# Optimization experiments

Hardware: AMD Instinct MI355X
Metric: run time of the kernel (lower is better)

Reference implementation:

```python
import jax, jax.numpy as jnp
import numpy as np

V = 32000; D = 128; L = 2048; B = 4
DI = 256; DS = 16; K = 4; H = 4; NM = 6; NA = 2; PAD = 0


def setup_inputs() -> dict:
    key = jax.random.key(0)
    ks = jax.random.split(key, 24)
    n = lambda i, shape, s: jax.random.normal(ks[i], shape, dtype=jnp.float32) * s
    inp = {}
    inp["input_ids"] = jax.random.randint(ks[0], (B, L), 0, V)
    inp["token_types"] = jax.random.randint(ks[1], (B, L), 0, 10)
    inp["timestamps"] = jax.random.uniform(ks[2], (B, L), dtype=jnp.float32)
    inp["emb"] = n(3, (V, D), 0.02).at[PAD].set(0.0)
    inp["type_emb"] = n(4, (10, D), 0.02)
    inp["te_freqs"] = n(5, (D // 2,), 0.1)
    inp["te_phases"] = jnp.zeros((D // 2,), jnp.float32)
    inp["te_w"] = n(6, (D, D), 0.05)
    inp["te_b"] = jnp.zeros((D,), jnp.float32)
    # Mamba blocks (stacked over NM)
    inp["m_norm_w"] = jnp.ones((NM, D), jnp.float32)
    inp["m_norm_b"] = jnp.zeros((NM, D), jnp.float32)
    inp["m_in_w"] = n(7, (NM, 2 * DI, D), 0.05)
    inp["m_conv_w"] = n(8, (NM, DI, 1, K), 0.2)   # depthwise, OIH with I=1
    inp["m_conv_b"] = jnp.zeros((NM, DI), jnp.float32)
    inp["m_dt_w"] = n(9, (NM, DI, DI), 0.05)
    inp["m_dt_b"] = jnp.zeros((NM, DI), jnp.float32)
    inp["m_B_w"] = n(10, (NM, DS, DI), 0.05)
    inp["m_C_w"] = n(11, (NM, DS, DI), 0.05)
    inp["m_D"] = jnp.ones((NM, DI), jnp.float32)
    inp["m_A_log"] = jnp.broadcast_to(jnp.log(jnp.arange(1, DS + 1, dtype=jnp.float32)), (NM, DI, DS)) + 0.0
    inp["m_out_w"] = n(12, (NM, D, DI), 0.05)
    # Attention blocks (stacked over NA)
    inp["a_ln1_w"] = jnp.ones((NA, D), jnp.float32)
    inp["a_ln1_b"] = jnp.zeros((NA, D), jnp.float32)
    inp["a_qkv_w"] = n(13, (NA, 3 * D, D), 0.05)
    inp["a_qkv_b"] = jnp.zeros((NA, 3 * D), jnp.float32)
    inp["a_out_w"] = n(14, (NA, D, D), 0.05)
    inp["a_out_b"] = jnp.zeros((NA, D), jnp.float32)
    inp["a_ln2_w"] = jnp.ones((NA, D), jnp.float32)
    inp["a_ln2_b"] = jnp.zeros((NA, D), jnp.float32)
    inp["a_f1_w"] = n(15, (NA, 4 * D, D), 0.05)
    inp["a_f1_b"] = jnp.zeros((NA, 4 * D), jnp.float32)
    inp["a_f2_w"] = n(16, (NA, D, 4 * D), 0.05)
    inp["a_f2_b"] = jnp.zeros((NA, D), jnp.float32)
    # Task head (n_tasks=1)
    inp["h_ln_w"] = jnp.ones((D,), jnp.float32)
    inp["h_ln_b"] = jnp.zeros((D,), jnp.float32)
    inp["h_w"] = n(17, (1, D), 0.05)
    inp["h_b"] = jnp.zeros((1,), jnp.float32)
    return inp


def _ln(x, w, b, eps=1e-5):
    mu = x.mean(-1, keepdims=True)
    var = ((x - mu) ** 2).mean(-1, keepdims=True)
    return (x - mu) * jax.lax.rsqrt(var + eps) * w + b


def _mamba(x, nw, nb, inw, cw, cb, dtw, dtb, bw, cpw, Dp, Alog, ow):
    res = x
    xn = _ln(x, nw, nb)
    xz = xn @ inw.T                              # [B,L,2*DI]
    xp, z = jnp.split(xz, 2, axis=-1)
    # causal depthwise conv: left-pad K-1, take first L outputs
    xc = jax.lax.conv_general_dilated(
        xp.transpose(0, 2, 1), cw, (1,), [(K - 1, 0)],
        feature_group_count=DI, dimension_numbers=("NCH", "OIH", "NCH"))
    xc = (xc + cb[None, :, None]).transpose(0, 2, 1)
    xc = jax.nn.silu(xc)
    dt = jax.nn.softplus(xc @ dtw.T + dtb)       # [B,L,DI]
    Bm = xc @ bw.T                               # [B,L,DS]
    Cm = xc @ cpw.T                              # [B,L,DS]
    A = -jnp.exp(Alog)                           # [DI,DS]

    def step(h, inp):
        dt_t, x_t, b_t, c_t = inp                # [B,DI],[B,DI],[B,DS],[B,DS]
        h = h * jnp.exp(A * dt_t[..., None]) + (x_t * dt_t)[..., None] * b_t[:, None, :]
        return h, (h * c_t[:, None, :]).sum(-1)

    xs = (jnp.moveaxis(dt, 1, 0), jnp.moveaxis(xc, 1, 0),
          jnp.moveaxis(Bm, 1, 0), jnp.moveaxis(Cm, 1, 0))
    h0 = jnp.zeros((x.shape[0], DI, DS), x.dtype)
    _, y = jax.lax.scan(step, h0, xs)            # y: [L,B,DI]
    y = jnp.moveaxis(y, 0, 1)
    y = y + xc * Dp
    y = y * jax.nn.silu(z)
    return res + y @ ow.T


def _attn(x, l1w, l1b, qkvw, qkvb, ow, ob, l2w, l2b, f1w, f1b, f2w, f2b):
    res = x
    xn = _ln(x, l1w, l1b)
    qkv = xn @ qkvw.T + qkvb
    q, k, v = jnp.split(qkv, 3, axis=-1)
    dh = D // H
    rs = lambda t: t.reshape(t.shape[0], t.shape[1], H, dh)
    q, k, v = rs(q), rs(k), rs(v)
    sc = jnp.einsum("bqhd,bkhd->bhqk", q, k) / jnp.sqrt(jnp.float32(dh))
    p = jax.nn.softmax(sc, axis=-1)
    o = jnp.einsum("bhqk,bkhd->bqhd", p, v).reshape(x.shape)
    x = res + o @ ow.T + ob
    ff = jax.nn.gelu(_ln(x, l2w, l2b) @ f1w.T + f1b, approximate=False) @ f2w.T + f2b
    return x + ff


def reference(input_ids, token_types, timestamps, emb, type_emb, te_freqs, te_phases, te_w, te_b,
              m_norm_w, m_norm_b, m_in_w, m_conv_w, m_conv_b, m_dt_w, m_dt_b, m_B_w, m_C_w,
              m_D, m_A_log, m_out_w,
              a_ln1_w, a_ln1_b, a_qkv_w, a_qkv_b, a_out_w, a_out_b, a_ln2_w, a_ln2_b,
              a_f1_w, a_f1_b, a_f2_w, a_f2_b, h_ln_w, h_ln_b, h_w, h_b):
    t = timestamps[..., None]
    enc = jnp.concatenate([jnp.sin(t * te_freqs + te_phases),
                           jnp.cos(t * te_freqs + te_phases)], axis=-1)
    x = emb[input_ids] + type_emb[token_types] + enc @ te_w.T + te_b
    attn_every = (NM + NA) // NA
    mi = 0; ai = 0
    for i in range(NM + NA):
        if (i + 1) % attn_every == 0:
            x = _attn(x, a_ln1_w[ai], a_ln1_b[ai], a_qkv_w[ai], a_qkv_b[ai],
                      a_out_w[ai], a_out_b[ai], a_ln2_w[ai], a_ln2_b[ai],
                      a_f1_w[ai], a_f1_b[ai], a_f2_w[ai], a_f2_b[ai])
            ai += 1
        else:
            x = _mamba(x, m_norm_w[mi], m_norm_b[mi], m_in_w[mi], m_conv_w[mi], m_conv_b[mi],
                       m_dt_w[mi], m_dt_b[mi], m_B_w[mi], m_C_w[mi], m_D[mi], m_A_log[mi], m_out_w[mi])
            mi += 1
    cls = x[:, 0, :]
    return (_ln(cls, h_ln_w, h_ln_b) @ h_w.T + h_b)[:, 0]
```

## Files before the change

### kernel.cpp

```cpp
#include <hip/hip_runtime.h>
#include <hip/hip_bf16.h>
#include <math.h>

constexpr int Ll = 2048, Bb = 4, DIi = 256, Hh = 4;
constexpr int TOK = Bb * Ll;
constexpr int NC = 128;
constexpr int CH = 16;
constexpr float LOG2E = 1.442695040888963f;

#define DEV __device__ __forceinline__

DEV float siluf(float v)     { return v / (1.f + expf(-v)); }
DEV float softplusf(float v) { return (v > 20.f) ? v : log1pf(expf(v)); }
DEV float geluf(float v)     { return 0.5f * v * (1.f + erff(v * 0.7071067811865476f)); }

#if defined(__has_builtin)
#if __has_builtin(__builtin_amdgcn_exp2f)
#define EXP2F __builtin_amdgcn_exp2f
#endif
#endif
#ifndef EXP2F
#define EXP2F exp2f
#endif

DEV short f2bf(float f) {
    union { float f; unsigned u; } a; a.f = f;
    unsigned r = (a.u + 0x7fffu + ((a.u >> 16) & 1u)) >> 16;
    return (short)r;
}

using bf16x8 = __attribute__((ext_vector_type(8))) short;
using f16x8  = __attribute__((ext_vector_type(8))) _Float16;
using f32x4  = __attribute__((ext_vector_type(4))) float;

__global__ __launch_bounds__(256) void wprep_kernel(
    const float* s0, const float* s1, const float* s2, const float* s3,
    const float* s4, const float* s5, const float* s6, const float* s7,
    const float* s8, const float* s9, _Float16* dst)
{
    constexpr int base[10] = {0, 16384, 409600, 802816, 827392, 851968,
                              1048576, 1146880, 1179648, 1310720};
    constexpr int nseg[10] = {16384, 393216, 393216, 24576, 24576, 196608,
                              98304, 32768, 131072, 131072};
    int seg = blockIdx.y;
    int t = blockIdx.x * 256 + threadIdx.x;
    if (t >= nseg[seg]) return;
    const float* src;
    switch (seg) {
        case 0: src = s0; break; case 1: src = s1; break;
        case 2: src = s2; break; case 3: src = s3; break;
        case 4: src = s4; break; case 5: src = s5; break;
        case 6: src = s6; break; case 7: src = s7; break;
        case 8: src = s8; break; default: src = s9; break;
    }
    dst[base[seg] + t] = (_Float16)src[t];
}

__global__ __launch_bounds__(256) void gather_enc_kernel(
    const int* __restrict__ ids, const int* __restrict__ tts,
    const float* __restrict__ ts, const float* __restrict__ emb,
    const float* __restrict__ temb, const float* __restrict__ freqs,
    const float* __restrict__ phases, float* __restrict__ x,
    float* __restrict__ enc)
{
    int tok = blockIdx.x * 2 + (threadIdx.x >> 7);
    int d = threadIdx.x & 127;
    float tval = ts[tok];
    int j = d & 63;
    float a = tval * freqs[j] + phases[j];
    enc[(size_t)tok * 128 + d] = (d < 64) ? sinf(a) : cosf(a);
    int id = ids[tok];
    int tt = tts[tok];
    x[(size_t)tok * 128 + d] = emb[(size_t)id * 128 + d] + temb[(size_t)tt * 128 + d];
}

__global__ __launch_bounds__(256) void ln_stats_kernel(
    const float* __restrict__ x, float2* __restrict__ stats)
{
    int wid = threadIdx.x >> 6, lane = threadIdx.x & 63;
    int tok = blockIdx.x * 4 + wid;
    float2 v = *(const float2*)(x + (size_t)tok * 128 + lane * 2);
    float s = v.x + v.y, sq = v.x * v.x + v.y * v.y;
#pragma unroll
    for (int o = 32; o > 0; o >>= 1) { s += __shfl_xor(s, o); sq += __shfl_xor(sq, o); }
    if (lane == 0) {
        float mu = s * (1.f / 128.f);
        float var = sq * (1.f / 128.f) - mu * mu;
        stats[tok] = make_float2(mu, rsqrtf(var + 1e-5f));
    }
}

template <int ACT, bool BIAS, bool ADD, bool LNA, int MODE>
__global__ __launch_bounds__(256) void gemm64_kernel(
    const float* __restrict__ A, const _Float16* __restrict__ W,
    const float* __restrict__ bias, float* __restrict__ C,
    const float* __restrict__ lnw, const float* __restrict__ lnb,
    const float2* __restrict__ stats,
    const _Float16* __restrict__ Bw, const _Float16* __restrict__ Cw,
    float* __restrict__ bmo, float* __restrict__ cmo,
    short* __restrict__ kbf, short* __restrict__ vbf,
    int M, int N, int Kd, int lda, int ldc)
{
    __shared__ _Float16 As[64][72];
    __shared__ _Float16 Ws[64][72];
    const int by = blockIdx.y;
    const bool isBC = (MODE == 1) && (by == (int)gridDim.y - 1);
    const int bm0 = blockIdx.x * 64, bn0 = by * 64;
    const int tid = threadIdx.x;
    const int w = tid >> 6, l = tid & 63;
    const int wr = w >> 1, wc = w & 1;
    const int fr = l & 15, fk = (l >> 4) * 8;
    const int srow = tid >> 2, skc = (tid & 3) * 16;
    float mu = 0.f, rstd = 1.f;
    if (LNA) { float2 st = stats[bm0 + srow]; mu = st.x; rstd = st.y; }
    f32x4 acc[2][2] = {};

    for (int k0 = 0; k0 < Kd; k0 += 64) {
        const float* ap = A + (size_t)(bm0 + srow) * lda + k0 + skc;
        const _Float16* wp;
        if (isBC) {
            if (srow < 16)      wp = Bw + (size_t)srow * Kd + k0 + skc;
            else if (srow < 32) wp = Cw + (size_t)(srow - 16) * Kd + k0 + skc;
            else                wp = Bw + k0 + skc;
        } else {
            wp = W + (size_t)(bn0 + srow) * Kd + k0 + skc;
        }
        float af[16];
#pragma unroll
        for (int q = 0; q < 4; q++)
            *(float4*)(af + q * 4) = *(const float4*)(ap + q * 4);
        f16x8 wb0 = *(const f16x8*)wp;
        f16x8 wb1 = *(const f16x8*)(wp + 8);
        if (LNA) {
#pragma unroll
            for (int q = 0; q < 4; q++) {
                float4 w4 = *(const float4*)(lnw + k0 + skc + q * 4);
                float4 b4 = *(const float4*)(lnb + k0 + skc + q * 4);
                af[q*4+0] = (af[q*4+0] - mu) * rstd * w4.x + b4.x;
                af[q*4+1] = (af[q*4+1] - mu) * rstd * w4.y + b4.y;
                af[q*4+2] = (af[q*4+2] - mu) * rstd * w4.z + b4.z;
                af[q*4+3] = (af[q*4+3] - mu) * rstd * w4.w + b4.w;
            }
        }
        f16x8 ab0, ab1;
#pragma unroll
        for (int q = 0; q < 8; q++) {
            ab0[q] = (_Float16)af[q]; ab1[q] = (_Float16)af[q + 8];
        }
        __syncthreads();
        *(f16x8*)&As[srow][skc]     = ab0;
        *(f16x8*)&As[srow][skc + 8] = ab1;
        *(f16x8*)&Ws[srow][skc]     = wb0;
        *(f16x8*)&Ws[srow][skc + 8] = wb1;
        __syncthreads();
#pragma unroll
        for (int ks = 0; ks < 64; ks += 32) {
            f16x8 afr0 = *(const f16x8*)&As[wr * 32 + fr][ks + fk];
            f16x8 afr1 = *(const f16x8*)&As[wr * 32 + 16 + fr][ks + fk];
            f16x8 wfr0 = *(const f16x8*)&Ws[wc * 32 + fr][ks + fk];
            f16x8 wfr1 = *(const f16x8*)&Ws[wc * 32 + 16 + fr][ks + fk];
            acc[0][0] = __builtin_amdgcn_mfma_f32_16x16x32_f16(afr0, wfr0, acc[0][0], 0, 0, 0);
            acc[0][1] = __builtin_amdgcn_mfma_f32_16x16x32_f16(afr0, wfr1, acc[0][1], 0, 0, 0);
            acc[1][0] = __builtin_amdgcn_mfma_f32_16x16x32_f16(afr1, wfr0, acc[1][0], 0, 0, 0);
            acc[1][1] = __builtin_amdgcn_mfma_f32_16x16x32_f16(afr1, wfr1, acc[1][1], 0, 0, 0);
        }
    }
#pragma unroll
    for (int ri = 0; ri < 2; ri++)
#pragma unroll
    for (int ci = 0; ci < 2; ci++) {
        const int lcol = wc * 32 + ci * 16 + fr;
        const int col = bn0 + lcol;
        const int row0 = bm0 + wr * 32 + ri * 16 + (l >> 4) * 4;
        if (isBC) {
            if (lcol < 32) {
                float* dst = (lcol < 16) ? bmo : cmo;
                const int cc = lcol & 15;
#pragma unroll
                for (int r = 0; r < 4; r++)
                    dst[(size_t)(row0 + r) * 16 + cc] = acc[ri][ci][r];
            }
        } else if (MODE == 2) {
            const float bv = bias[col];
            const int b = row0 >> 11, tl0 = row0 & 2047;
            if (col < 128) {
#pragma unroll
                for (int r = 0; r < 4; r++)
                    C[(size_t)(row0 + r) * 128 + col] = acc[ri][ci][r] + bv;
            } else if (col < 256) {
                const int hc = col - 128;
                short* kp = kbf + ((size_t)(b * 4 + (hc >> 5)) * 2048 + tl0) * 32 + (hc & 31);
#pragma unroll
                for (int r = 0; r < 4; r++)
                    kp[(size_t)r * 32] = f2bf(acc[ri][ci][r] + bv);
            } else {
                const int hc = col - 256;
                short4 vk;
#pragma unroll
                for (int r = 0; r < 4; r++)
                    ((short*)&vk)[r] = f2bf(acc[ri][ci][r] + bv);
                *(short4*)(vbf + ((size_t)(b * 4 + (hc >> 5)) * 32 + (hc & 31)) * 2048 + tl0) = vk;
            }
        } else {
            const float bv = BIAS ? bias[col] : 0.f;
#pragma unroll
            for (int r = 0; r < 4; r++) {
                float t = acc[ri][ci][r] + bv;
                if (ACT == 1) t = softplusf(t);
                if (ACT == 2) t = geluf(t);
                float* p = C + (size_t)(row0 + r) * ldc + col;
                if (ADD) t += *p;
                *p = t;
            }
        }
    }
}

__global__ __launch_bounds__(256) void conv_kernel(
    const float* __restrict__ xz, const float* __restrict__ cw,
    const float* __restrict__ cb, float* __restrict__ xc)
{
    int g = blockIdx.x * 256 + threadIdx.x;
    int c = g & 255;
    int t = (g >> 8) & 2047;
    int b = g >> 19;
    float4 w4 = *(const float4*)(cw + (size_t)c * 4);
    float acc = cb[c];
    const float* base = xz + ((size_t)b * 2048 + t) * 512 + c;
    if (t >= 3) {
        acc += base[-3 * 512] * w4.x + base[-2 * 512] * w4.y + base[-512] * w4.z + base[0] * w4.w;
    } else {
        const float wv[4] = {w4.x, w4.y, w4.z, w4.w};
#pragma unroll
        for (int kk = 0; kk < 4; kk++) {
            int tt = t - 3 + kk;
            if (tt >= 0) acc += xz[((size_t)b * 2048 + tt) * 512 + c] * wv[kk];
        }
    }
    xc[g] = siluf(acc);
}

__global__ __launch_bounds__(256) void scan1_kernel(
    const float* __restrict__ dt, const float* __restrict__ xc,
    const float* __restrict__ bm, const float* __restrict__ Alog,
    float* __restrict__ F, float* __restrict__ sumdt)
{
    int c = threadIdx.x;
    int k = blockIdx.x & (NC - 1);
    int b = blockIdx.x / NC;
    __shared__ float sB[CH][16];
    int t0 = k * CH;
    if (threadIdx.x < CH * 4) {
        int r = threadIdx.x >> 2, c4 = (threadIdx.x & 3) << 2;
        *(float4*)&sB[r][c4] = *(const float4*)(bm + ((size_t)b * 2048 + t0 + r) * 16 + c4);
    }
    float A2[16];
#pragma unroll
    for (int s = 0; s < 16; s++) A2[s] = -expf(Alog[(size_t)c * 16 + s]) * LOG2E;
    __syncthreads();
    float h[16] = {};
    float sd = 0.f;
    size_t base = ((size_t)b * 2048 + t0) * 256 + c;
    for (int tt = 0; tt < CH; tt++) {
        float d  = dt[base + (size_t)tt * 256];
        float xv = xc[base + (size_t)tt * 256];
        sd += d;
        float xdt = xv * d;
#pragma unroll
        for (int s = 0; s < 16; s++) h[s] = h[s] * EXP2F(A2[s] * d) + xdt * sB[tt][s];
    }
    size_t fo = (((size_t)b * NC + k) * 256 + c) * 16;
#pragma unroll
    for (int s = 0; s < 16; s += 4) *(float4*)(F + fo + s) = make_float4(h[s], h[s+1], h[s+2], h[s+3]);
    sumdt[((size_t)b * NC + k) * 256 + c] = sd;
}

__global__ __launch_bounds__(256) void scan2_kernel(
    float* __restrict__ F, const float* __restrict__ sumdt,
    const float* __restrict__ Alog)
{
    int g = blockIdx.x * 256 + threadIdx.x;
    int s = g & 15, c = (g >> 4) & 255, b = g >> 12;
    float A2 = -expf(Alog[(size_t)c * 16 + s]) * LOG2E;
    float h = 0.f;
    for (int k = 0; k < NC; k++) {
        size_t o = (((size_t)b * NC + k) * 256 + c) * 16 + s;
        float tmp = F[o];
        F[o] = h;
        h = h * EXP2F(A2 * sumdt[((size_t)b * NC + k) * 256 + c]) + tmp;
    }
}

__global__ __launch_bounds__(256) void scan3_kernel(
    const float* __restrict__ dt, const float* __restrict__ xc,
    const float* __restrict__ bm, const float* __restrict__ cm,
    const float* __restrict__ xz, const float* __restrict__ Alog,
    const float* __restrict__ Dp, const float* __restrict__ Hs,
    float* __restrict__ y)
{
    int c = threadIdx.x;
    int k = blockIdx.x & (NC - 1);
    int b = blockIdx.x / NC;
    __shared__ float sB[CH][16], sC[CH][16];
    int t0 = k * CH;
    if (threadIdx.x < CH * 4) {
        int r = threadIdx.x >> 2, c4 = (threadIdx.x & 3) << 2;
        *(float4*)&sB[r][c4] = *(const float4*)(bm + ((size_t)b * 2048 + t0 + r) * 16 + c4);
        *(float4*)&sC[r][c4] = *(const float4*)(cm + ((size_t)b * 2048 + t0 + r) * 16 + c4);
    }
    float A2[16];
#pragma unroll
    for (int s = 0; s < 16; s++) A2[s] = -expf(Alog[(size_t)c * 16 + s]) * LOG2E;
    __syncthreads();
    float h[16];
    size_t ho = (((size_t)b * NC + k) * 256 + c) * 16;
#pragma unroll
    for (int s = 0; s < 16; s++) h[s] = Hs[ho + s];
    float Dv = Dp[c];
    size_t base  = ((size_t)b * 2048 + t0) * 256 + c;
    size_t zbase = ((size_t)b * 2048 + t0) * 512 + 256 + c;
    for (int tt = 0; tt < CH; tt++) {
        float d  = dt[base + (size_t)tt * 256];
        float xv = xc[base + (size_t)tt * 256];
        float xdt = xv * d;
        float yv = 0.f;
#pragma unroll
        for (int s = 0; s < 16; s++) {
            h[s] = h[s] * EXP2F(A2[s] * d) + xdt * sB[tt][s];
            yv += h[s] * sC[tt][s];
        }
        yv += xv * Dv;
        float zv = xz[zbase + (size_t)tt * 512];
        y[base + (size_t)tt * 256] = yv * siluf(zv);
    }
}

__global__ __launch_bounds__(256) void attn_part_kernel(
    const float* __restrict__ qbuf, const short* __restrict__ kbf,
    const short* __restrict__ vbf, float* __restrict__ pO, float* __restrict__ pml)
{
    __shared__ short Klds[2][64 * 32];
    __shared__ short Vlds[2][32 * 64];
    __shared__ short Pt[4][64][18];
    const int qt = blockIdx.x, b = blockIdx.z;
    const int h = blockIdx.y >> 2, sp = blockIdx.y & 3;
    const int tid = threadIdx.x;
    const int w = tid >> 6, l = tid & 63;
    const int q16 = l & 15, g = l >> 4;
    const float cQ = 0.25503634043f;

    const int qrow = qt * 64 + w * 16 + q16;
    const float* qp = qbuf + ((size_t)(b * 2048 + qrow)) * 128 + 32 * h + g * 8;
    bf16x8 qfrag;
    {
        float qf[8];
        *(float4*)qf       = *(const float4*)qp;
        *(float4*)(qf + 4) = *(const float4*)(qp + 4);
#pragma unroll
        for (int i = 0; i < 8; i++) qfrag[i] = f2bf(qf[i] * cQ);
    }
    const int bh = b * 4 + h;
    const short* kb = kbf + ((size_t)bh * 2048) * 32;
    const short* vb = vbf + ((size_t)bh * 32) * 2048;

    const int vrow = tid >> 3;
    const int vsw  = ((tid & 7) * 16) ^ ((vrow & 7) << 4);
    const int ts0 = sp * 8;

    bf16x8 kst, vst;
    auto ldregs = [&](int t) {
        kst = *(const bf16x8*)(kb + (size_t)t * 2048 + tid * 8);
        vst = *(const bf16x8*)(vb + (size_t)vrow * 2048 + t * 64 + (vsw >> 1));
    };
    auto dswrite = [&](int buf) {
        *(bf16x8*)&Klds[buf][tid * 8] = kst;
        *(bf16x8*)&Vlds[buf][tid * 8] = vst;
    };

    float m = -1e30f, lsum = 0.f;
    f32x4 O0 = {0.f, 0.f, 0.f, 0.f}, O1 = {0.f, 0.f, 0.f, 0.f};
    const f32x4 zf = {0.f, 0.f, 0.f, 0.f};

    auto step = [&](int buf) {
        bf16x8 kf[4];
#pragma unroll
        for (int kt = 0; kt < 4; kt++)
            kf[kt] = *(const bf16x8*)&Klds[buf][(kt * 16 + q16) * 32 + g * 8];
        f32x4 St[4];
#pragma unroll
        for (int kt = 0; kt < 4; kt++)
            St[kt] = __builtin_amdgcn_mfma_f32_16x16x32_bf16(kf[kt], qfrag, zf, 0, 0, 0);
        float pm = St[0][0];
#pragma unroll
        for (int kt = 0; kt < 4; kt++)
#pragma unroll
            for (int r = 0; r < 4; r++) pm = fmaxf(pm, St[kt][r]);
        pm = fmaxf(pm, __shfl_xor(pm, 16));
        pm = fmaxf(pm, __shfl_xor(pm, 32));
        float mn = fmaxf(m, pm);
        float rs = EXP2F(m - mn);
        float ps = 0.f;
#pragma unroll
        for (int kt = 0; kt < 4; kt++)
#pragma unroll
            for (int r = 0; r < 4; r++) {
                float p = EXP2F(St[kt][r] - mn);
                ps += p;
                Pt[w][kt * 16 + g * 4 + r][q16] = f2bf(p);
            }
        ps += __shfl_xor(ps, 16);
        ps += __shfl_xor(ps, 32);
        lsum = lsum * rs + ps;
        m = mn;
        O0 *= rs; O1 *= rs;
#pragma unroll
        for (int c = 0; c < 2; c++) {
            bf16x8 pb;
#pragma unroll
            for (int i = 0; i < 8; i++) pb[i] = Pt[w][c * 32 + g * 8 + i][q16];
#pragma unroll
            for (int hf = 0; hf < 2; hf++) {
                const int d = q16 + 16 * hf;
                bf16x8 vf = *(const bf16x8*)&Vlds[buf][d * 64 + ((c * 32 + g * 8) ^ ((d & 7) << 3))];
                if (hf == 0) O0 = __builtin_amdgcn_mfma_f32_16x16x32_bf16(vf, pb, O0, 0, 0, 0);
                else         O1 = __builtin_amdgcn_mfma_f32_16x16x32_bf16(vf, pb, O1, 0, 0, 0);
            }
        }
    };

    ldregs(ts0);
    dswrite(0);
    ldregs(ts0 + 1);
    int cur = 0;
    for (int i = 0; i < 8; i++) {
        __syncthreads();
        if (i + 1 < 8) {
            dswrite(cur ^ 1);
            if (i + 2 < 8) ldregs(ts0 + i + 2);
        }
        step(cur);
        cur ^= 1;
    }

    size_t po = (((size_t)(bh * 4 + sp)) * 2048 + qrow) * 32;
#pragma unroll
    for (int r = 0; r < 4; r++) {
        pO[po + g * 4 + r]      = O0[r];
        pO[po + 16 + g * 4 + r] = O1[r];
    }
    if (g == 0) {
        size_t mo = (((size_t)(bh * 4 + sp)) * 2048 + qrow) * 2;
        pml[mo]     = m;
        pml[mo + 1] = lsum;
    }
}

__global__ __launch_bounds__(256) void attn_comb_kernel(
    const float* __restrict__ pO, const float* __restrict__ pml,
    float* __restrict__ aout)
{
    int gid = blockIdx.x * 256 + threadIdx.x;
    int d = gid & 31, q = (gid >> 5) & 2047, bh = gid >> 16;
    float m[4], lv[4], M = -1e30f;
#pragma unroll
    for (int s = 0; s < 4; s++) {
        size_t mo = (((size_t)(bh * 4 + s)) * 2048 + q) * 2;
        m[s] = pml[mo]; lv[s] = pml[mo + 1];
        M = fmaxf(M, m[s]);
    }
    float L = 0.f, o = 0.f;
#pragma unroll
    for (int s = 0; s < 4; s++) {
        float wgt = EXP2F(m[s] - M);
        L += lv[s] * wgt;
        o += pO[(((size_t)(bh * 4 + s)) * 2048 + q) * 32 + d] * wgt;
    }
    int b = bh >> 2, h = bh & 3;
    aout[((size_t)(b * 2048 + q)) * 128 + h * 32 + d] = o / L;
}

__global__ __launch_bounds__(128) void head_kernel(
    const float* __restrict__ x, const float* __restrict__ w,
    const float* __restrict__ bsp, const float* __restrict__ hw,
    const float* __restrict__ hb, float* __restrict__ out)
{
    int bb = blockIdx.x;
    int d = threadIdx.x;
    int wid = d >> 6, lane = d & 63;
    float v = x[(size_t)bb * 2048 * 128 + d];
    float s = v, sq = v * v;
#pragma unroll
    for (int o = 32; o > 0; o >>= 1) { s += __shfl_xor(s, o); sq += __shfl_xor(sq, o); }
    __shared__ float red[4];
    if (lane == 0) { red[wid] = s; red[2 + wid] = sq; }
    __syncthreads();
    s = red[0] + red[1]; sq = red[2] + red[3];
    float mu = s * (1.f / 128.f);
    float var = sq * (1.f / 128.f) - mu * mu;
    float xn = (v - mu) * rsqrtf(var + 1e-5f) * w[d] + bsp[d];
    float pr = xn * hw[d];
#pragma unroll
    for (int o = 32; o > 0; o >>= 1) pr += __shfl_xor(pr, o);
    __syncthreads();
    if (lane == 0) red[wid] = pr;
    __syncthreads();
    if (d == 0) out[bb] = red[0] + red[1] + hb[0];
}

constexpr size_t OFF_X  = 0;
constexpr size_t OFF_XZ = (size_t)1 << 20;
constexpr size_t OFF_XC = (size_t)5 << 20;
constexpr size_t OFF_DT = (size_t)7 << 20;
constexpr size_t OFF_Y  = (size_t)9 << 20;
constexpr size_t OFF_BM = (size_t)11 << 20;
constexpr size_t OFF_CM = OFF_BM + 131072;
constexpr size_t OFF_SD = OFF_CM + 131072;
constexpr size_t OFF_ST = OFF_SD + 131072;
constexpr size_t OFF_F  = OFF_ST + 16384;
constexpr size_t OFF_WF = OFF_F + ((size_t)2 << 20);
constexpr size_t WS_FLOATS = OFF_WF + 720896;

extern "C" void kernel_launch(void* const* d_in, const int* in_sizes, int n_in,
                              void* d_out, int out_size, void* d_ws, size_t ws_size,
                              hipStream_t stream)
{
    const int*   ids   = (const int*)d_in[0];
    const int*   tts   = (const int*)d_in[1];
    const float* tstmp = (const float*)d_in[2];
    const float* emb   = (const float*)d_in[3];
    const float* temb  = (const float*)d_in[4];
    const float* tef   = (const float*)d_in[5];
    const float* tep   = (const float*)d_in[6];
    const float* tew   = (const float*)d_in[7];
    const float* tebi  = (const float*)d_in[8];
    const float* mnw   = (const float*)d_in[9];
    const float* mnb   = (const float*)d_in[10];
    const float* minw  = (const float*)d_in[11];
    const float* mcwp  = (const float*)d_in[12];
    const float* mcb   = (const float*)d_in[13];
    const float* mdtw  = (const float*)d_in[14];
    const float* mdtb  = (const float*)d_in[15];
    const float* mbw   = (const float*)d_in[16];
    const float* mcw2  = (const float*)d_in[17];
    const float* mD    = (const float*)d_in[18];
    const float* mAl   = (const float*)d_in[19];
    const float* mow   = (const float*)d_in[20];
    const float* al1w  = (const float*)d_in[21];
    const float* al1b  = (const float*)d_in[22];
    const float* aqkvw = (const float*)d_in[23];
    const float* aqkvb = (const float*)d_in[24];
    const float* aow   = (const float*)d_in[25];
    const float* aob   = (const float*)d_in[26];
    const float* al2w  = (const float*)d_in[27];
    const float* al2b  = (const float*)d_in[28];
    const float* af1w  = (const float*)d_in[29];
    const float* af1b  = (const float*)d_in[30];
    const float* af2w  = (const float*)d_in[31];
    const float* af2b  = (const float*)d_in[32];
    const float* hlnw  = (const float*)d_in[33];
    const float* hlnb  = (const float*)d_in[34];
    const float* hw    = (const float*)d_in[35];
    const float* hb    = (const float*)d_in[36];
    float* out = (float*)d_out;
    float* wsf = (float*)d_ws;
    if (ws_size < WS_FLOATS * sizeof(float)) return;

    float* x    = wsf + OFF_X;
    float* xz   = wsf + OFF_XZ;
    float* xc   = wsf + OFF_XC;
    float* dtb  = wsf + OFF_DT;
    float* yb   = wsf + OFF_Y;
    float* bm   = wsf + OFF_BM;
    float* cm   = wsf + OFF_CM;
    float* sdb  = wsf + OFF_SD;
    float2* stats = (float2*)(wsf + OFF_ST);
    float* Fb   = wsf + OFF_F;
    float* ff   = xz;
    float* aout = yb;
    float* qbuf = xc;
    float* pO   = xz;
    float* pml  = dtb;
    float* encb = Fb;
    short* kbf  = (short*)(wsf + OFF_F);
    short* vbf  = (short*)(wsf + OFF_F + ((size_t)1 << 20));
    _Float16* wf16 = (_Float16*)(wsf + OFF_WF);

    const _Float16* tew16   = wf16;
    const _Float16* minw16  = wf16 + 16384;
    const _Float16* mdtw16  = wf16 + 409600;
    const _Float16* mbw16   = wf16 + 802816;
    const _Float16* mcw216  = wf16 + 827392;
    const _Float16* mow16   = wf16 + 851968;
    const _Float16* aqkvw16 = wf16 + 1048576;
    const _Float16* aow16   = wf16 + 1146880;
    const _Float16* af1w16  = wf16 + 1179648;
    const _Float16* af2w16  = wf16 + 1310720;

    wprep_kernel<<<dim3(1536, 10), 256, 0, stream>>>(
        tew, minw, mdtw, mbw, mcw2, mow, aqkvw, aow, af1w, af2w, wf16);

    gather_enc_kernel<<<TOK / 2, 256, 0, stream>>>(ids, tts, tstmp, emb, temb, tef, tep, x, encb);
    gemm64_kernel<0, true, true, false, 0><<<dim3(128, 2), 256, 0, stream>>>(
        encb, tew16, tebi, x, nullptr, nullptr, nullptr, nullptr, nullptr,
        nullptr, nullptr, nullptr, nullptr, TOK, 128, 128, 128, 128);

    int mi = 0, ai = 0;
    for (int i = 0; i < 8; i++) {
        if ((i + 1) % 4 == 0) {
            ln_stats_kernel<<<TOK / 4, 256, 0, stream>>>(x, stats);
            gemm64_kernel<0, true, false, true, 2><<<dim3(128, 6), 256, 0, stream>>>(
                x, aqkvw16 + (size_t)ai * 49152, aqkvb + ai * 384, qbuf,
                al1w + ai * 128, al1b + ai * 128, stats, nullptr, nullptr,
                nullptr, nullptr, kbf, vbf, TOK, 384, 128, 128, 128);
            attn_part_kernel<<<dim3(32, 16, Bb), 256, 0, stream>>>(qbuf, kbf, vbf, pO, pml);
            attn_comb_kernel<<<4096, 256, 0, stream>>>(pO, pml, aout);
            gemm64_kernel<0, true, true, false, 0><<<dim3(128, 2), 256, 0, stream>>>(
                aout, aow16 + (size_t)ai * 16384, aob + ai * 128, x,
                nullptr, nullptr, nullptr, nullptr, nullptr,
                nullptr, nullptr, nullptr, nullptr, TOK, 128, 128, 128, 128);
            ln_stats_kernel<<<TOK / 4, 256, 0, stream>>>(x, stats);
            gemm64_kernel<2, true, false, true, 0><<<dim3(128, 8), 256, 0, stream>>>(
                x, af1w16 + (size_t)ai * 65536, af1b + ai * 512, ff,
                al2w + ai * 128, al2b + ai * 128, stats, nullptr, nullptr,
                nullptr, nullptr, nullptr, nullptr, TOK, 512, 128, 128, 512);
            gemm64_kernel<0, true, true, false, 0><<<dim3(128, 2), 256, 0, stream>>>(
                ff, af2w16 + (size_t)ai * 65536, af2b + ai * 128, x,
                nullptr, nullptr, nullptr, nullptr, nullptr,
                nullptr, nullptr, nullptr, nullptr, TOK, 128, 512, 512, 128);
            ai++;
        } else {
            const float* Al = mAl + (size_t)mi * DIi * 16;
            ln_stats_kernel<<<TOK / 4, 256, 0, stream>>>(x, stats);
            gemm64_kernel<0, false, false, true, 0><<<dim3(128, 8), 256, 0, stream>>>(
                x, minw16 + (size_t)mi * 65536, nullptr, xz,
                mnw + mi * 128, mnb + mi * 128, stats, nullptr, nullptr,
                nullptr, nullptr, nullptr, nullptr, TOK, 512, 128, 128, 512);
            conv_kernel<<<8192, 256, 0, stream>>>(xz, mcwp + (size_t)mi * DIi * 4, mcb + mi * DIi, xc);
            gemm64_kernel<1, true, false, false, 1><<<dim3(128, 5), 256, 0, stream>>>(
                xc, mdtw16 + (size_t)mi * 65536, mdtb + mi * 256, dtb,
                nullptr, nullptr, nullptr,
                mbw16 + (size_t)mi * 4096, mcw216 + (size_t)mi * 4096,
                bm, cm, nullptr, nullptr, TOK, 256, 256, 256, 256);
            scan1_kernel<<<Bb * NC, 256, 0, stream>>>(dtb, xc, bm, Al, Fb, sdb);
            scan2_kernel<<<64, 256, 0, stream>>>(Fb, sdb, Al);
            scan3_kernel<<<Bb * NC, 256, 0, stream>>>(dtb, xc, bm, cm, xz, Al, mD + mi * 256, Fb, yb);
            gemm64_kernel<0, false, true, false, 0><<<dim3(128, 2), 256, 0, stream>>>(
                yb, mow16 + (size_t)mi * 32768, nullptr, x,
                nullptr, nullptr, nullptr, nullptr, nullptr,
                nullptr, nullptr, nullptr, nullptr, TOK, 128, 256, 256, 128);
            mi++;
        }
    }
    head_kernel<<<Bb, 128, 0, stream>>>(x, hlnw, hlnb, hw, hb, out);
}
```

Measured before the change: 695.0 us.

## Fuse LayerNorm stats into LN-prologue GEMMs and vectorize depthwise conv

Drops the separate ln_stats kernel. LN-prologue GEMMs now load the full K=128 row into registers, reduce mean and variance with lane shuffles, and process the whole K in a single LDS stage with a wider padded tile. This removes 10 kernel launches and one re-read of x per LN, at the cost of N/64-fold redundant stats computation per row and more registers and LDS per block. The conv kernel now handles four channels per thread with float4 loads and stores, using a quarter of the launch grid.

```diff
diff --git a/kernel.cpp b/kernel.cpp
--- a/kernel.cpp
+++ b/kernel.cpp
@@ -74,35 +74,21 @@
     x[(size_t)tok * 128 + d] = emb[(size_t)id * 128 + d] + temb[(size_t)tt * 128 + d];
 }
 
-__global__ __launch_bounds__(256) void ln_stats_kernel(
-    const float* __restrict__ x, float2* __restrict__ stats)
-{
-    int wid = threadIdx.x >> 6, lane = threadIdx.x & 63;
-    int tok = blockIdx.x * 4 + wid;
-    float2 v = *(const float2*)(x + (size_t)tok * 128 + lane * 2);
-    float s = v.x + v.y, sq = v.x * v.x + v.y * v.y;
-#pragma unroll
-    for (int o = 32; o > 0; o >>= 1) { s += __shfl_xor(s, o); sq += __shfl_xor(sq, o); }
-    if (lane == 0) {
-        float mu = s * (1.f / 128.f);
-        float var = sq * (1.f / 128.f) - mu * mu;
-        stats[tok] = make_float2(mu, rsqrtf(var + 1e-5f));
-    }
-}
-
 template <int ACT, bool BIAS, bool ADD, bool LNA, int MODE>
 __global__ __launch_bounds__(256) void gemm64_kernel(
     const float* __restrict__ A, const _Float16* __restrict__ W,
     const float* __restrict__ bias, float* __restrict__ C,
     const float* __restrict__ lnw, const float* __restrict__ lnb,
-    const float2* __restrict__ stats,
     const _Float16* __restrict__ Bw, const _Float16* __restrict__ Cw,
     float* __restrict__ bmo, float* __restrict__ cmo,
     short* __restrict__ kbf, short* __restrict__ vbf,
     int M, int N, int Kd, int lda, int ldc)
 {
-    __shared__ _Float16 As[64][72];
-    __shared__ _Float16 Ws[64][72];
+    constexpr int PADK = LNA ? 136 : 72;
+    __shared__ _Float16 As[64][PADK];
+    __shared__ _Float16 Ws[64][PADK];
+    __shared__ float sMu[LNA ? 64 : 1];
+    __shared__ float sRs[LNA ? 64 : 1];
     const int by = blockIdx.y;
     const bool isBC = (MODE == 1) && (by == (int)gridDim.y - 1);
     const int bm0 = blockIdx.x * 64, bn0 = by * 64;
@@ -110,51 +96,50 @@
     const int w = tid >> 6, l = tid & 63;
     const int wr = w >> 1, wc = w & 1;
     const int fr = l & 15, fk = (l >> 4) * 8;
-    const int srow = tid >> 2, skc = (tid & 3) * 16;
-    float mu = 0.f, rstd = 1.f;
-    if (LNA) { float2 st = stats[bm0 + srow]; mu = st.x; rstd = st.y; }
+    const int srow = tid >> 2;
     f32x4 acc[2][2] = {};
 
-    for (int k0 = 0; k0 < Kd; k0 += 64) {
-        const float* ap = A + (size_t)(bm0 + srow) * lda + k0 + skc;
-        const _Float16* wp;
-        if (isBC) {
-            if (srow < 16)      wp = Bw + (size_t)srow * Kd + k0 + skc;
-            else if (srow < 32) wp = Cw + (size_t)(srow - 16) * Kd + k0 + skc;
-            else                wp = Bw + k0 + skc;
-        } else {
-            wp = W + (size_t)(bn0 + srow) * Kd + k0 + skc;
-        }
-        float af[16];
-#pragma unroll
-        for (int q = 0; q < 4; q++)
-            *(float4*)(af + q * 4) = *(const float4*)(ap + q * 4);
-        f16x8 wb0 = *(const f16x8*)wp;
-        f16x8 wb1 = *(const f16x8*)(wp + 8);
-        if (LNA) {
-#pragma unroll
-            for (int q = 0; q < 4; q++) {
-                float4 w4 = *(const float4*)(lnw + k0 + skc + q * 4);
-                float4 b4 = *(const float4*)(lnb + k0 + skc + q * 4);
-                af[q*4+0] = (af[q*4+0] - mu) * rstd * w4.x + b4.x;
-                af[q*4+1] = (af[q*4+1] - mu) * rstd * w4.y + b4.y;
-                af[q*4+2] = (af[q*4+2] - mu) * rstd * w4.z + b4.z;
-                af[q*4+3] = (af[q*4+3] - mu) * rstd * w4.w + b4.w;
-            }
-        }
-        f16x8 ab0, ab1;
-#pragma unroll
-        for (int q = 0; q < 8; q++) {
-            ab0[q] = (_Float16)af[q]; ab1[q] = (_Float16)af[q + 8];
-        }
+    if (LNA) {
+        const int kofs = (tid & 3) * 32;
+        const float* ap = A + (size_t)(bm0 + srow) * lda + kofs;
+        float av[32];
+#pragma unroll
+        for (int q = 0; q < 8; q++)
+            *(float4*)(av + q * 4) = *(const float4*)(ap + q * 4);
+        float s = 0.f, sq = 0.f;
+#pragma unroll
+        for (int q = 0; q < 32; q++) { s += av[q]; sq += av[q] * av[q]; }
+        s  += __shfl_xor(s, 1);  s  += __shfl_xor(s, 2);
+        sq += __shfl_xor(sq, 1); sq += __shfl_xor(sq, 2);
+        if ((tid & 3) == 0) {
+            float mu = s * (1.f / 128.f);
+            float var = sq * (1.f / 128.f) - mu * mu;
+            sMu[srow] = mu;
+            sRs[srow] = rsqrtf(var + 1e-5f);
+        }
+        const _Float16* wp = W + (size_t)(bn0 + srow) * Kd + kofs;
+        f16x8 wv0 = *(const f16x8*)wp,        wv1 = *(const f16x8*)(wp + 8);
+        f16x8 wv2 = *(const f16x8*)(wp + 16), wv3 = *(const f16x8*)(wp + 24);
         __syncthreads();
-        *(f16x8*)&As[srow][skc]     = ab0;
-        *(f16x8*)&As[srow][skc + 8] = ab1;
-        *(f16x8*)&Ws[srow][skc]     = wb0;
-        *(f16x8*)&Ws[srow][skc + 8] = wb1;
+        float mu = sMu[srow], rs = sRs[srow];
+#pragma unroll
+        for (int v = 0; v < 4; v++) {
+            f16x8 a16;
+#pragma unroll
+            for (int j = 0; j < 8; j++) {
+                float g = lnw[kofs + v * 8 + j];
+                float bb = lnb[kofs + v * 8 + j];
+                a16[j] = (_Float16)((av[v * 8 + j] - mu) * rs * g + bb);
+            }
+            *(f16x8*)&As[srow][kofs + v * 8] = a16;
+        }
+        *(f16x8*)&Ws[srow][kofs]      = wv0;
+        *(f16x8*)&Ws[srow][kofs + 8]  = wv1;
+        *(f16x8*)&Ws[srow][kofs + 16] = wv2;
+        *(f16x8*)&Ws[srow][kofs + 24] = wv3;
         __syncthreads();
 #pragma unroll
-        for (int ks = 0; ks < 64; ks += 32) {
+        for (int ks = 0; ks < 128; ks += 32) {
             f16x8 afr0 = *(const f16x8*)&As[wr * 32 + fr][ks + fk];
             f16x8 afr1 = *(const f16x8*)&As[wr * 32 + 16 + fr][ks + fk];
             f16x8 wfr0 = *(const f16x8*)&Ws[wc * 32 + fr][ks + fk];
@@ -164,6 +149,47 @@
             acc[1][0] = __builtin_amdgcn_mfma_f32_16x16x32_f16(afr1, wfr0, acc[1][0], 0, 0, 0);
             acc[1][1] = __builtin_amdgcn_mfma_f32_16x16x32_f16(afr1, wfr1, acc[1][1], 0, 0, 0);
         }
+    } else {
+        const int skc = (tid & 3) * 16;
+        for (int k0 = 0; k0 < Kd; k0 += 64) {
+            const float* ap = A + (size_t)(bm0 + srow) * lda + k0 + skc;
+            const _Float16* wp;
+            if (isBC) {
+                if (srow < 16)      wp = Bw + (size_t)srow * Kd + k0 + skc;
+                else if (srow < 32) wp = Cw + (size_t)(srow - 16) * Kd + k0 + skc;
+                else                wp = Bw + k0 + skc;
+            } else {
+                wp = W + (size_t)(bn0 + srow) * Kd + k0 + skc;
+            }
+            float af[16];
+#pragma unroll
+            for (int q = 0; q < 4; q++)
+                *(float4*)(af + q * 4) = *(const float4*)(ap + q * 4);
+            f16x8 wb0 = *(const f16x8*)wp;
+            f16x8 wb1 = *(const f16x8*)(wp + 8);
+            f16x8 ab0, ab1;
+#pragma unroll
+            for (int q = 0; q < 8; q++) {
+                ab0[q] = (_Float16)af[q]; ab1[q] = (_Float16)af[q + 8];
+            }
+            __syncthreads();
+            *(f16x8*)&As[srow][skc]     = ab0;
+            *(f16x8*)&As[srow][skc + 8] = ab1;
+            *(f16x8*)&Ws[srow][skc]     = wb0;
+            *(f16x8*)&Ws[srow][skc + 8] = wb1;
+            __syncthreads();
+#pragma unroll
+            for (int ks = 0; ks < 64; ks += 32) {
+                f16x8 afr0 = *(const f16x8*)&As[wr * 32 + fr][ks + fk];
+                f16x8 afr1 = *(const f16x8*)&As[wr * 32 + 16 + fr][ks + fk];
+                f16x8 wfr0 = *(const f16x8*)&Ws[wc * 32 + fr][ks + fk];
+                f16x8 wfr1 = *(const f16x8*)&Ws[wc * 32 + 16 + fr][ks + fk];
+                acc[0][0] = __builtin_amdgcn_mfma_f32_16x16x32_f16(afr0, wfr0, acc[0][0], 0, 0, 0);
+                acc[0][1] = __builtin_amdgcn_mfma_f32_16x16x32_f16(afr0, wfr1, acc[0][1], 0, 0, 0);
+                acc[1][0] = __builtin_amdgcn_mfma_f32_16x16x32_f16(afr1, wfr0, acc[1][0], 0, 0, 0);
+                acc[1][1] = __builtin_amdgcn_mfma_f32_16x16x32_f16(afr1, wfr1, acc[1][1], 0, 0, 0);
+            }
+        }
     }
 #pragma unroll
     for (int ri = 0; ri < 2; ri++)
@@ -221,23 +247,29 @@
     const float* __restrict__ cb, float* __restrict__ xc)
 {
     int g = blockIdx.x * 256 + threadIdx.x;
-    int c = g & 255;
-    int t = (g >> 8) & 2047;
-    int b = g >> 19;
-    float4 w4 = *(const float4*)(cw + (size_t)c * 4);
-    float acc = cb[c];
-    const float* base = xz + ((size_t)b * 2048 + t) * 512 + c;
-    if (t >= 3) {
-        acc += base[-3 * 512] * w4.x + base[-2 * 512] * w4.y + base[-512] * w4.z + base[0] * w4.w;
-    } else {
-        const float wv[4] = {w4.x, w4.y, w4.z, w4.w};
-#pragma unroll
-        for (int kk = 0; kk < 4; kk++) {
-            int tt = t - 3 + kk;
-            if (tt >= 0) acc += xz[((size_t)b * 2048 + tt) * 512 + c] * wv[kk];
-        }
-    }
-    xc[g] = siluf(acc);
+    int c4 = g & 63;
+    int t  = (g >> 6) & 2047;
+    int b  = g >> 17;
+    int c  = c4 * 4;
+    float4 w0 = *(const float4*)(cw + (size_t)c * 4);
+    float4 w1 = *(const float4*)(cw + (size_t)(c + 1) * 4);
+    float4 w2 = *(const float4*)(cw + (size_t)(c + 2) * 4);
+    float4 w3 = *(const float4*)(cw + (size_t)(c + 3) * 4);
+    float4 bi = *(const float4*)(cb + c);
+    float4 xk[4];
+#pragma unroll
+    for (int kk = 0; kk < 4; kk++) {
+        int tt = t - 3 + kk;
+        if (tt >= 0) xk[kk] = *(const float4*)(xz + ((size_t)b * 2048 + tt) * 512 + c);
+        else xk[kk] = make_float4(0.f, 0.f, 0.f, 0.f);
+    }
+    float4 r;
+    r.x = bi.x + xk[0].x * w0.x + xk[1].x * w0.y + xk[2].x * w0.z + xk[3].x * w0.w;
+    r.y = bi.y + xk[0].y * w1.x + xk[1].y * w1.y + xk[2].y * w1.z + xk[3].y * w1.w;
+    r.z = bi.z + xk[0].z * w2.x + xk[1].z * w2.y + xk[2].z * w2.z + xk[3].z * w2.w;
+    r.w = bi.w + xk[0].w * w3.x + xk[1].w * w3.y + xk[2].w * w3.z + xk[3].w * w3.w;
+    r.x = siluf(r.x); r.y = siluf(r.y); r.z = siluf(r.z); r.w = siluf(r.w);
+    *(float4*)(xc + ((size_t)b * 2048 + t) * 256 + c) = r;
 }
 
 __global__ __launch_bounds__(256) void scan1_kernel(
@@ -573,7 +605,6 @@
     float* bm   = wsf + OFF_BM;
     float* cm   = wsf + OFF_CM;
     float* sdb  = wsf + OFF_SD;
-    float2* stats = (float2*)(wsf + OFF_ST);
     float* Fb   = wsf + OFF_F;
     float* ff   = xz;
     float* aout = yb;
@@ -601,44 +632,41 @@
 
     gather_enc_kernel<<<TOK / 2, 256, 0, stream>>>(ids, tts, tstmp, emb, temb, tef, tep, x, encb);
     gemm64_kernel<0, true, true, false, 0><<<dim3(128, 2), 256, 0, stream>>>(
-        encb, tew16, tebi, x, nullptr, nullptr, nullptr, nullptr, nullptr,
+        encb, tew16, tebi, x, nullptr, nullptr, nullptr, nullptr,
         nullptr, nullptr, nullptr, nullptr, TOK, 128, 128, 128, 128);
 
     int mi = 0, ai = 0;
     for (int i = 0; i < 8; i++) {
         if ((i + 1) % 4 == 0) {
-            ln_stats_kernel<<<TOK / 4, 256, 0, stream>>>(x, stats);
             gemm64_kernel<0, true, false, true, 2><<<dim3(128, 6), 256, 0, stream>>>(
                 x, aqkvw16 + (size_t)ai * 49152, aqkvb + ai * 384, qbuf,
-                al1w + ai * 128, al1b + ai * 128, stats, nullptr, nullptr,
+                al1w + ai * 128, al1b + ai * 128, nullptr, nullptr,
                 nullptr, nullptr, kbf, vbf, TOK, 384, 128, 128, 128);
             attn_part_kernel<<<dim3(32, 16, Bb), 256, 0, stream>>>(qbuf, kbf, vbf, pO, pml);
             attn_comb_kernel<<<4096, 256, 0, stream>>>(pO, pml, aout);
             gemm64_kernel<0, true, true, false, 0><<<dim3(128, 2), 256, 0, stream>>>(
                 aout, aow16 + (size_t)ai * 16384, aob + ai * 128, x,
-                nullptr, nullptr, nullptr, nullptr, nullptr,
+                nullptr, nullptr, nullptr, nullptr,
                 nullptr, nullptr, nullptr, nullptr, TOK, 128, 128, 128, 128);
-            ln_stats_kernel<<<TOK / 4, 256, 0, stream>>>(x, stats);
             gemm64_kernel<2, true, false, true, 0><<<dim3(128, 8), 256, 0, stream>>>(
                 x, af1w16 + (size_t)ai * 65536, af1b + ai * 512, ff,
-                al2w + ai * 128, al2b + ai * 128, stats, nullptr, nullptr,
+                al2w + ai * 128, al2b + ai * 128, nullptr, nullptr,
                 nullptr, nullptr, nullptr, nullptr, TOK, 512, 128, 128, 512);
             gemm64_kernel<0, true, true, false, 0><<<dim3(128, 2), 256, 0, stream>>>(
                 ff, af2w16 + (size_t)ai * 65536, af2b + ai * 128, x,
-                nullptr, nullptr, nullptr, nullptr, nullptr,
+                nullptr, nullptr, nullptr, nullptr,
                 nullptr, nullptr, nullptr, nullptr, TOK, 128, 512, 512, 128);
             ai++;
         } else {
             const float* Al = mAl + (size_t)mi * DIi * 16;
-            ln_stats_kernel<<<TOK / 4, 256, 0, stream>>>(x, stats);
             gemm64_kernel<0, false, false, true, 0><<<dim3(128, 8), 256, 0, stream>>>(
                 x, minw16 + (size_t)mi * 65536, nullptr, xz,
-                mnw + mi * 128, mnb + mi * 128, stats, nullptr, nullptr,
+                mnw + mi * 128, mnb + mi * 128, nullptr, nullptr,
                 nullptr, nullptr, nullptr, nullptr, TOK, 512, 128, 128, 512);
-            conv_kernel<<<8192, 256, 0, stream>>>(xz, mcwp + (size_t)mi * DIi * 4, mcb + mi * DIi, xc);
+            conv_kernel<<<2048, 256, 0, stream>>>(xz, mcwp + (size_t)mi * DIi * 4, mcb + mi * DIi, xc);
             gemm64_kernel<1, true, false, false, 1><<<dim3(128, 5), 256, 0, stream>>>(
                 xc, mdtw16 + (size_t)mi * 65536, mdtb + mi * 256, dtb,
-                nullptr, nullptr, nullptr,
+                nullptr, nullptr,
                 mbw16 + (size_t)mi * 4096, mcw216 + (size_t)mi * 4096,
                 bm, cm, nullptr, nullptr, TOK, 256, 256, 256, 256);
             scan1_kernel<<<Bb * NC, 256, 0, stream>>>(dtb, xc, bm, Al, Fb, sdb);
@@ -646,7 +674,7 @@
             scan3_kernel<<<Bb * NC, 256, 0, stream>>>(dtb, xc, bm, cm, xz, Al, mD + mi * 256, Fb, yb);
             gemm64_kernel<0, false, true, false, 0><<<dim3(128, 2), 256, 0, stream>>>(
                 yb, mow16 + (size_t)mi * 32768, nullptr, x,
-                nullptr, nullptr, nullptr, nullptr, nullptr,
+                nullptr, nullptr, nullptr, nullptr,
                 nullptr, nullptr, nullptr, nullptr, TOK, 128, 256, 256, 128);
             mi++;
         }
```

Result: slower. 714.1 us (+2.8%).
